# Kernel optimization log

Measured on AMD Instinct MI355X. Metric: run time of the kernel, lower is better.

The kernel has to match this reference:

```python
import jax, jax.numpy as jnp
import numpy as np
from functools import partial

# --- config (matches init_kwargs cfg) ---
MAX_OBS = 16
MAX_AGENTS = 9
NA = MAX_AGENTS - 1            # 8 neighbor agents
NC = MAX_OBS + 2 * NA          # 32 HOCBF constraint rows
A_MAX = 1.0
W_MAX = 1.0
D_MAX = 10.0
D_OBS = 0.5
D_SAFE = 0.5
DAMPING = 2.0
STIFFNESS = 1.0
W_SLACK = 100.0
B = 65536
N_ITERS = 100   # ADMM iterations for the batched QP solve
RHO = 1.0


def setup_inputs() -> dict:
    key = jax.random.key(0)
    k = jax.random.split(key, 8)
    return {
        "u_nominal": jax.random.normal(k[0], (B, 2), dtype=jnp.float32),
        "v_current": jax.random.uniform(k[1], (B, 1), dtype=jnp.float32),
        "p_obs": jax.random.normal(k[2], (B, MAX_OBS, 2), dtype=jnp.float32),
        "p_agents": jax.random.normal(k[3], (B, NA, 2), dtype=jnp.float32),
        "v_agents_local": jax.random.normal(k[4], (B, NA, 2), dtype=jnp.float32),
        "agent_active": jnp.ones((B, NA), dtype=jnp.float32),
        "obs_active": jnp.ones((B, MAX_OBS), dtype=jnp.float32),
    }


def _build_Gh(v_current, p_obs, p_agents, v_agents_local, agent_active, obs_active):
    """Faithful translation of the G/h constraint construction."""
    # obstacle CBF rows  (v_current is (B,1) and broadcasts against (B,MAX_OBS))
    lx_o, ly_o = p_obs[..., 0], p_obs[..., 1]
    h_obs = lx_o ** 2 + ly_o ** 2 - D_OBS ** 2
    h_dot_obs = -2.0 * lx_o * v_current
    G_obs = jnp.stack([2.0 * lx_o,
                       2.0 * ly_o * v_current,
                       -jnp.ones_like(lx_o)], axis=-1)           # (B, MAX_OBS, 3)
    h_obs_row = (2.0 * v_current ** 2 + DAMPING * h_dot_obs
                 + STIFFNESS * h_obs) * obs_active               # (B, MAX_OBS)

    # inter-agent avoidance rows
    lx_a, ly_a = p_agents[..., 0], p_agents[..., 1]
    v_jx, v_jy = v_agents_local[..., 0], v_agents_local[..., 1]
    h_avoid = lx_a ** 2 + ly_a ** 2 - D_SAFE ** 2
    h_dot_avoid = -2.0 * lx_a * v_current + 2.0 * (lx_a * v_jx + ly_a * v_jy)
    G_av_a = 2.0 * lx_a
    G_av_w = 2.0 * ly_a * v_current - 2.0 * ly_a * v_jx + 2.0 * lx_a * v_jy
    h_ddot_c = (2.0 * v_current ** 2 - 2.0 * v_current * v_jx
                + 2.0 * (-v_current * v_jx + v_jx ** 2 + v_jy ** 2))
    G_avoid = jnp.stack([G_av_a * agent_active,
                         G_av_w * agent_active,
                         jnp.zeros_like(lx_a)], axis=-1)         # (B, NA, 3)
    h_avoid_row = (h_ddot_c + DAMPING * h_dot_avoid + STIFFNESS * h_avoid) * agent_active

    # connectivity rows
    h_conn = D_MAX ** 2 - (lx_a ** 2 + ly_a ** 2)
    h_dot_conn = -h_dot_avoid
    G_conn = jnp.stack([-G_av_a * agent_active,
                        -G_av_w * agent_active,
                        jnp.zeros_like(lx_a)], axis=-1)          # (B, NA, 3)
    h_conn_row = (-h_ddot_c + DAMPING * h_dot_conn + STIFFNESS * h_conn) * agent_active

    G = jnp.concatenate([G_obs, G_avoid, G_conn], axis=1)        # (B, NC, 3)
    h = jnp.concatenate([h_obs_row, h_avoid_row, h_conn_row], axis=1)  # (B, NC)
    return G, h


def _solve_qp(u_ref, G, h):
    """Batched ADMM solve of: min ||u - u_ref||^2 + w_slack*delta^2,
    s.t. [G; box] x <= [h; box_b], x = [u1, u2, delta]."""
    Bn = u_ref.shape[0]
    box_A = jnp.array([[-1., 0., 0.], [1., 0., 0.],
                       [0., -1., 0.], [0., 1., 0.],
                       [0., 0., -1.]], dtype=u_ref.dtype)
    box_b = jnp.array([A_MAX, A_MAX, W_MAX, W_MAX, 0.0], dtype=u_ref.dtype)
    A = jnp.concatenate([G, jnp.broadcast_to(box_A, (Bn, 5, 3))], axis=1)  # (B, m, 3)
    b = jnp.concatenate([h, jnp.broadcast_to(box_b, (Bn, 5))], axis=1)     # (B, m)

    Q = jnp.diag(jnp.array([2.0, 2.0, 2.0 * W_SLACK], dtype=u_ref.dtype))
    q = jnp.concatenate([-2.0 * u_ref, jnp.zeros((Bn, 1), u_ref.dtype)], axis=1)

    M = Q + RHO * jnp.einsum('bki,bkj->bij', A, A)   # (B, 3, 3)
    Minv = jnp.linalg.inv(M)

    def step(carry, _):
        x, z, y = carry
        rhs = -q + jnp.einsum('bkj,bk->bj', A, RHO * z - y)
        x = jnp.einsum('bij,bj->bi', Minv, rhs)
        v = jnp.einsum('bkj,bj->bk', A, x)
        z = jnp.minimum(v + y / RHO, b)
        y = y + RHO * (v - z)
        return (x, z, y), None

    x0 = jnp.zeros((Bn, 3), u_ref.dtype)
    z0 = jnp.minimum(jnp.zeros_like(b), b)
    y0 = jnp.zeros_like(b)
    (x, _, _), _ = jax.lax.scan(step, (x0, z0, y0), None, length=N_ITERS)
    return x


def reference(u_nominal, v_current, p_obs, p_agents, v_agents_local,
              agent_active, obs_active):
    action_scale = jnp.array([A_MAX, W_MAX], dtype=u_nominal.dtype)
    u_ref = u_nominal * action_scale
    G, h = _build_Gh(v_current, p_obs, p_agents, v_agents_local,
                     agent_active, obs_active)
    x = _solve_qp(u_ref, G, h)      # (B, 3) = [u1, u2, delta]
    u_safe = x[:, :2] / action_scale
    return u_safe
```

## Files before the change

kernel.cpp:

```cpp
#include <hip/hip_runtime.h>


constexpr int NOBS = 16;
constexpr int NAG  = 8;
constexpr int NITERS = 100;

typedef float v2 __attribute__((ext_vector_type(2)));

static __device__ __forceinline__ v2 vfma(v2 a, v2 b, v2 c) { return __builtin_elementwise_fma(a, b, c); }
static __device__ __forceinline__ v2 vmax(v2 a, v2 b)       { return __builtin_elementwise_max(a, b); }
static __device__ __forceinline__ v2 vabs(v2 a)             { return __builtin_elementwise_abs(a); }

__global__ __launch_bounds__(256, 1)
void cbf_admm_kernel(const float* __restrict__ u_nom,
                     const float* __restrict__ v_cur,
                     const float* __restrict__ p_obs,
                     const float* __restrict__ p_ag,
                     const float* __restrict__ v_ag,
                     const float* __restrict__ ag_act,
                     const float* __restrict__ ob_act,
                     float* __restrict__ out,
                     int B)
{
    const int b = blockIdx.x * blockDim.x + threadIdx.x;
    if (b >= B) return;

    const float v   = v_cur[b];
    const float2 un = *reinterpret_cast<const float2*>(u_nom + 2 * (size_t)b);
    const float ur0 = un.x;
    const float ur1 = un.y;

    v2 ga2[8], gw2[8], h2[8];
    {
        const float4* po = reinterpret_cast<const float4*>(p_obs + (size_t)b * 2 * NOBS);
        const float2* oa = reinterpret_cast<const float2*>(ob_act + (size_t)b * NOBS);
        #pragma unroll
        for (int q = 0; q < 8; ++q) {
            const float4 p  = po[q];
            const float2 ac = oa[q];
            const v2 lx = {p.x, p.z};
            const v2 ly = {p.y, p.w};
            const v2 act = {ac.x, ac.y};
            ga2[q] = 2.f * lx;
            gw2[q] = (2.f * v) * ly;
            const v2 h_obs = lx * lx + ly * ly - 0.25f;
            const v2 hdot  = (-2.f * v) * lx;
            h2[q] = (2.f * v * v + 2.f * hdot + h_obs) * act;
        }
    }

    v2 gaa2[4], gwa2[4], hav2[4], hcn2[4];
    {
        const float4* pa  = reinterpret_cast<const float4*>(p_ag  + (size_t)b * 2 * NAG);
        const float4* va  = reinterpret_cast<const float4*>(v_ag  + (size_t)b * 2 * NAG);
        const float2* aa  = reinterpret_cast<const float2*>(ag_act + (size_t)b * NAG);
        #pragma unroll
        for (int q = 0; q < 4; ++q) {
            const float4 p  = pa[q];
            const float4 w4 = va[q];
            const float2 ac = aa[q];
            const v2 lx = {p.x,  p.z},  ly = {p.y,  p.w};
            const v2 vx = {w4.x, w4.z}, vy = {w4.y, w4.w};
            const v2 act = {ac.x, ac.y};
            const v2 d2  = lx * lx + ly * ly;
            const v2 h_avoid = d2 - 0.25f;
            const v2 hdot = (-2.f * v) * lx + 2.f * (lx * vx + ly * vy);
            const v2 hddc = (2.f * v * v) + (-4.f * v) * vx + 2.f * (vx * vx + vy * vy);
            const v2 Ga = 2.f * lx;
            const v2 Gw = (2.f * v) * ly - 2.f * ly * vx + 2.f * lx * vy;
            gaa2[q] = Ga * act;
            gwa2[q] = Gw * act;
            hav2[q] = (hddc + 2.f * hdot + h_avoid) * act;
            hcn2[q] = (-hddc - 2.f * hdot + (100.f - d2)) * act;
        }
    }

    v2 m00 = {4.f, 0.f}, m01 = {0.f, 0.f}, m11 = {4.f, 0.f}, m02 = {0.f, 0.f}, m12 = {0.f, 0.f};
    #pragma unroll
    for (int q = 0; q < 8; ++q) {
        m00 = vfma(ga2[q], ga2[q], m00);
        m01 = vfma(ga2[q], gw2[q], m01);
        m11 = vfma(gw2[q], gw2[q], m11);
        m02 = m02 - ga2[q];
        m12 = m12 - gw2[q];
    }
    #pragma unroll
    for (int q = 0; q < 4; ++q) {
        const v2 two = {2.f, 2.f};
        m00 = vfma(two * gaa2[q], gaa2[q], m00);
        m01 = vfma(two * gaa2[q], gwa2[q], m01);
        m11 = vfma(two * gwa2[q], gwa2[q], m11);
    }
    const float M00 = m00.x + m00.y, M01 = m01.x + m01.y, M11 = m11.x + m11.y;
    const float M02 = m02.x + m02.y, M12 = m12.x + m12.y;
    const float M22 = 217.f;
    const float c00 = M11 * M22 - M12 * M12;
    const float c01 = M02 * M12 - M01 * M22;
    const float c02 = M01 * M12 - M02 * M11;
    const float det = M00 * c00 + M01 * c01 + M02 * c02;
    const float id  = 1.f / det;
    const float i00 = c00 * id, i01 = c01 * id, i02 = c02 * id;
    const float i11 = (M00 * M22 - M02 * M02) * id;
    const float i12 = (M01 * M02 - M00 * M12) * id;
    const float i22 = (M00 * M11 - M01 * M01) * id;

    const v2 Z = {0.f, 0.f};
    v2 w2[8], wav2[4], wcn2[4];
    #pragma unroll
    for (int q = 0; q < 8; ++q) w2[q] = __builtin_elementwise_min(Z, h2[q]);
    #pragma unroll
    for (int q = 0; q < 4; ++q) {
        wav2[q] = __builtin_elementwise_min(Z, hav2[q]);
        wcn2[q] = __builtin_elementwise_min(Z, hcn2[q]);
    }
    v2 wb01 = Z, wb23 = Z;
    float wb4 = 0.f;
    const v2 ONE = {1.f, 1.f};

    float x0 = 0.f, x1 = 0.f, x2 = 0.f;

    #pragma unroll 1
    for (int it = 0; it < NITERS; ++it) {
        v2 a0 = Z, a1 = Z, a2 = Z;
        v2 dobs[8], dav[4], dcn[4];
        #pragma unroll
        for (int q = 0; q < 8; ++q) {
            const v2 d = w2[q] - h2[q];
            dobs[q] = d;
            const v2 t = h2[q] - vabs(d);
            a0 = vfma(ga2[q], t, a0);
            a1 = vfma(gw2[q], t, a1);
            a2 = a2 - t;
        }
        #pragma unroll
        for (int q = 0; q < 4; ++q) {
            const v2 da = wav2[q] - hav2[q];  dav[q] = da;
            const v2 dc = wcn2[q] - hcn2[q];  dcn[q] = dc;
            const v2 ta = hav2[q] - vabs(da);
            const v2 tc = hcn2[q] - vabs(dc);
            const v2 td = ta - tc;
            a0 = vfma(gaa2[q], td, a0);
            a1 = vfma(gwa2[q], td, a1);
        }
        const v2 db01 = wb01 - ONE, db23 = wb23 - ONE;
        const v2 tb01 = ONE - vabs(db01), tb23 = ONE - vabs(db23);
        const float tb4 = -fabsf(wb4);

        const float r0 = 2.f * ur0 + a0.x + a0.y + (tb01.y - tb01.x);
        const float r1 = 2.f * ur1 + a1.x + a1.y + (tb23.y - tb23.x);
        const float r2 = a2.x + a2.y - tb4;

        x0 = fmaf(i00, r0, fmaf(i01, r1, i02 * r2));
        x1 = fmaf(i01, r0, fmaf(i11, r1, i12 * r2));
        x2 = fmaf(i02, r0, fmaf(i12, r1, i22 * r2));

        const v2 X0 = {x0, x0}, X1 = {x1, x1}, NX2 = {-x2, -x2};
        #pragma unroll
        for (int q = 0; q < 8; ++q) {
            const v2 vv = vfma(ga2[q], X0, vfma(gw2[q], X1, NX2));
            w2[q] = vv + vmax(dobs[q], Z);
        }
        #pragma unroll
        for (int q = 0; q < 4; ++q) {
            const v2 va = vfma(gaa2[q], X0, gwa2[q] * X1);
            wav2[q] = va + vmax(dav[q], Z);
            wcn2[q] = vmax(dcn[q], Z) - va;
        }
        const v2 sx0 = {-x0, x0}, sx1 = {-x1, x1};
        wb01 = sx0 + vmax(db01, Z);
        wb23 = sx1 + vmax(db23, Z);
        wb4  = -x2 + fmaxf(wb4, 0.f);
    }

    reinterpret_cast<float2*>(out)[b] = make_float2(x0, x1);
}

extern "C" void kernel_launch(void* const* d_in, const int* in_sizes, int n_in,
                              void* d_out, int out_size, void* d_ws, size_t ws_size,
                              hipStream_t stream) {
    const float* u_nom  = (const float*)d_in[0];
    const float* v_cur  = (const float*)d_in[1];
    const float* p_obs  = (const float*)d_in[2];
    const float* p_ag   = (const float*)d_in[3];
    const float* v_ag   = (const float*)d_in[4];
    const float* ag_act = (const float*)d_in[5];
    const float* ob_act = (const float*)d_in[6];
    float* out = (float*)d_out;

    const int B = in_sizes[1];
    dim3 block(256), grid((B + 255) / 256);
    hipLaunchKernelGGL(cbf_admm_kernel, grid, block, 0, stream,
                       u_nom, v_cur, p_obs, p_ag, v_ag, ag_act, ob_act, out, B);
}
```

Measured before the change: 49.67 us.

## Split each QP across two lanes with DPP lane-swap reductions

Each batch element is now handled by two adjacent threads, each owning half of the constraint rows. Partial sums for the ADMM right-hand side and the M matrix are combined every iteration with a DPP quad-permute lane swap, and the box constraints are split between the two lanes. Launch bounds move to two blocks per CU and the grid doubles. This is meant to raise parallelism and occupancy for B=65536, since one thread per element gives only 256 blocks. The cost is duplicated 3x3 solve work and a lane exchange on the serial per-iteration dependency chain.

```diff
diff --git a/kernel.cpp b/kernel.cpp
--- a/kernel.cpp
+++ b/kernel.cpp
@@ -1,17 +1,20 @@
 #include <hip/hip_runtime.h>
 
 
-constexpr int NOBS = 16;
-constexpr int NAG  = 8;
 constexpr int NITERS = 100;
 
 typedef float v2 __attribute__((ext_vector_type(2)));
 
 static __device__ __forceinline__ v2 vfma(v2 a, v2 b, v2 c) { return __builtin_elementwise_fma(a, b, c); }
 static __device__ __forceinline__ v2 vmax(v2 a, v2 b)       { return __builtin_elementwise_max(a, b); }
+static __device__ __forceinline__ v2 vmin(v2 a, v2 b)       { return __builtin_elementwise_min(a, b); }
 static __device__ __forceinline__ v2 vabs(v2 a)             { return __builtin_elementwise_abs(a); }
 
-__global__ __launch_bounds__(256, 1)
+static __device__ __forceinline__ float lane_swap(float x) {
+    return __int_as_float(__builtin_amdgcn_mov_dpp(__float_as_int(x), 0xB1, 0xF, 0xF, true));
+}
+
+__global__ __launch_bounds__(256, 2)
 void cbf_admm_kernel(const float* __restrict__ u_nom,
                      const float* __restrict__ v_cur,
                      const float* __restrict__ p_obs,
@@ -22,25 +25,28 @@
                      float* __restrict__ out,
                      int B)
 {
-    const int b = blockIdx.x * blockDim.x + threadIdx.x;
-    if (b >= B) return;
-
-    const float v   = v_cur[b];
-    const float2 un = *reinterpret_cast<const float2*>(u_nom + 2 * (size_t)b);
+    const int t  = blockIdx.x * blockDim.x + threadIdx.x;
+    const int e  = t >> 1;
+    const int hf = t & 1;
+    if (e >= B) return;
+
+    const float v   = v_cur[e];
+    const float2 un = *reinterpret_cast<const float2*>(u_nom + 2 * (size_t)e);
     const float ur0 = un.x;
     const float ur1 = un.y;
 
-    v2 ga2[8], gw2[8], h2[8];
+    v2 ga2[4], gw2[4], h2[4];
     {
-        const float4* po = reinterpret_cast<const float4*>(p_obs + (size_t)b * 2 * NOBS);
-        const float2* oa = reinterpret_cast<const float2*>(ob_act + (size_t)b * NOBS);
-        #pragma unroll
-        for (int q = 0; q < 8; ++q) {
-            const float4 p  = po[q];
-            const float2 ac = oa[q];
+        const float4* po = reinterpret_cast<const float4*>(p_obs) + 4 * (size_t)t;
+        const float4* oa = reinterpret_cast<const float4*>(ob_act) + 2 * (size_t)t;
+        const float4 A0 = oa[0], A1 = oa[1];
+        const float oaf[8] = {A0.x, A0.y, A0.z, A0.w, A1.x, A1.y, A1.z, A1.w};
+        #pragma unroll
+        for (int q = 0; q < 4; ++q) {
+            const float4 p = po[q];
             const v2 lx = {p.x, p.z};
             const v2 ly = {p.y, p.w};
-            const v2 act = {ac.x, ac.y};
+            const v2 act = {oaf[2 * q], oaf[2 * q + 1]};
             ga2[q] = 2.f * lx;
             gw2[q] = (2.f * v) * ly;
             const v2 h_obs = lx * lx + ly * ly - 0.25f;
@@ -49,19 +55,19 @@
         }
     }
 
-    v2 gaa2[4], gwa2[4], hav2[4], hcn2[4];
+    v2 gaa2[2], gwa2[2], hav2[2], hcn2[2];
     {
-        const float4* pa  = reinterpret_cast<const float4*>(p_ag  + (size_t)b * 2 * NAG);
-        const float4* va  = reinterpret_cast<const float4*>(v_ag  + (size_t)b * 2 * NAG);
-        const float2* aa  = reinterpret_cast<const float2*>(ag_act + (size_t)b * NAG);
-        #pragma unroll
-        for (int q = 0; q < 4; ++q) {
+        const float4* pa = reinterpret_cast<const float4*>(p_ag) + 2 * (size_t)t;
+        const float4* va = reinterpret_cast<const float4*>(v_ag) + 2 * (size_t)t;
+        const float4 AA  = reinterpret_cast<const float4*>(ag_act)[t];
+        const float aaf[4] = {AA.x, AA.y, AA.z, AA.w};
+        #pragma unroll
+        for (int q = 0; q < 2; ++q) {
             const float4 p  = pa[q];
             const float4 w4 = va[q];
-            const float2 ac = aa[q];
             const v2 lx = {p.x,  p.z},  ly = {p.y,  p.w};
             const v2 vx = {w4.x, w4.z}, vy = {w4.y, w4.w};
-            const v2 act = {ac.x, ac.y};
+            const v2 act = {aaf[2 * q], aaf[2 * q + 1]};
             const v2 d2  = lx * lx + ly * ly;
             const v2 h_avoid = d2 - 0.25f;
             const v2 hdot = (-2.f * v) * lx + 2.f * (lx * vx + ly * vy);
@@ -75,9 +81,9 @@
         }
     }
 
-    v2 m00 = {4.f, 0.f}, m01 = {0.f, 0.f}, m11 = {4.f, 0.f}, m02 = {0.f, 0.f}, m12 = {0.f, 0.f};
-    #pragma unroll
-    for (int q = 0; q < 8; ++q) {
+    v2 m00 = {0.f, 0.f}, m01 = m00, m11 = m00, m02 = m00, m12 = m00;
+    #pragma unroll
+    for (int q = 0; q < 4; ++q) {
         m00 = vfma(ga2[q], ga2[q], m00);
         m01 = vfma(ga2[q], gw2[q], m01);
         m11 = vfma(gw2[q], gw2[q], m11);
@@ -85,14 +91,19 @@
         m12 = m12 - gw2[q];
     }
     #pragma unroll
-    for (int q = 0; q < 4; ++q) {
-        const v2 two = {2.f, 2.f};
-        m00 = vfma(two * gaa2[q], gaa2[q], m00);
-        m01 = vfma(two * gaa2[q], gwa2[q], m01);
-        m11 = vfma(two * gwa2[q], gwa2[q], m11);
-    }
-    const float M00 = m00.x + m00.y, M01 = m01.x + m01.y, M11 = m11.x + m11.y;
-    const float M02 = m02.x + m02.y, M12 = m12.x + m12.y;
+    for (int q = 0; q < 2; ++q) {
+        const v2 g2 = gaa2[q] + gaa2[q];
+        m00 = vfma(g2, gaa2[q], m00);
+        m01 = vfma(g2, gwa2[q], m01);
+        m11 = vfma(gwa2[q] + gwa2[q], gwa2[q], m11);
+    }
+    float pM00 = m00.x + m00.y, pM01 = m01.x + m01.y, pM11 = m11.x + m11.y;
+    float pM02 = m02.x + m02.y, pM12 = m12.x + m12.y;
+    const float M00 = pM00 + lane_swap(pM00) + 4.f;
+    const float M01 = pM01 + lane_swap(pM01);
+    const float M11 = pM11 + lane_swap(pM11) + 4.f;
+    const float M02 = pM02 + lane_swap(pM02);
+    const float M12 = pM12 + lane_swap(pM12);
     const float M22 = 217.f;
     const float c00 = M11 * M22 - M12 * M12;
     const float c01 = M02 * M12 - M01 * M22;
@@ -105,35 +116,35 @@
     const float i22 = (M00 * M11 - M01 * M01) * id;
 
     const v2 Z = {0.f, 0.f};
-    v2 w2[8], wav2[4], wcn2[4];
-    #pragma unroll
-    for (int q = 0; q < 8; ++q) w2[q] = __builtin_elementwise_min(Z, h2[q]);
-    #pragma unroll
-    for (int q = 0; q < 4; ++q) {
-        wav2[q] = __builtin_elementwise_min(Z, hav2[q]);
-        wcn2[q] = __builtin_elementwise_min(Z, hcn2[q]);
-    }
-    v2 wb01 = Z, wb23 = Z;
+    const v2 ONE = {1.f, 1.f};
+    v2 w2[4], wav2[2], wcn2[2];
+    #pragma unroll
+    for (int q = 0; q < 4; ++q) w2[q] = vmin(Z, h2[q]);
+    #pragma unroll
+    for (int q = 0; q < 2; ++q) {
+        wav2[q] = vmin(Z, hav2[q]);
+        wcn2[q] = vmin(Z, hcn2[q]);
+    }
+    v2 wbp = Z;
     float wb4 = 0.f;
-    const v2 ONE = {1.f, 1.f};
 
     float x0 = 0.f, x1 = 0.f, x2 = 0.f;
 
     #pragma unroll 1
     for (int it = 0; it < NITERS; ++it) {
-        v2 a0 = Z, a1 = Z, a2 = Z;
-        v2 dobs[8], dav[4], dcn[4];
-        #pragma unroll
-        for (int q = 0; q < 8; ++q) {
+        v2 a0 = Z, a1 = Z, tsum = Z;
+        v2 dobs[4], dav[2], dcn[2];
+        #pragma unroll
+        for (int q = 0; q < 4; ++q) {
             const v2 d = w2[q] - h2[q];
             dobs[q] = d;
-            const v2 t = h2[q] - vabs(d);
-            a0 = vfma(ga2[q], t, a0);
-            a1 = vfma(gw2[q], t, a1);
-            a2 = a2 - t;
-        }
-        #pragma unroll
-        for (int q = 0; q < 4; ++q) {
+            const v2 tt = h2[q] - vabs(d);
+            a0 = vfma(ga2[q], tt, a0);
+            a1 = vfma(gw2[q], tt, a1);
+            tsum = tsum + tt;
+        }
+        #pragma unroll
+        for (int q = 0; q < 2; ++q) {
             const v2 da = wav2[q] - hav2[q];  dav[q] = da;
             const v2 dc = wcn2[q] - hcn2[q];  dcn[q] = dc;
             const v2 ta = hav2[q] - vabs(da);
@@ -142,13 +153,20 @@
             a0 = vfma(gaa2[q], td, a0);
             a1 = vfma(gwa2[q], td, a1);
         }
-        const v2 db01 = wb01 - ONE, db23 = wb23 - ONE;
-        const v2 tb01 = ONE - vabs(db01), tb23 = ONE - vabs(db23);
-        const float tb4 = -fabsf(wb4);
-
-        const float r0 = 2.f * ur0 + a0.x + a0.y + (tb01.y - tb01.x);
-        const float r1 = 2.f * ur1 + a1.x + a1.y + (tb23.y - tb23.x);
-        const float r2 = a2.x + a2.y - tb4;
+        const v2 db = wbp - ONE;
+        const v2 tb = ONE - vabs(db);
+        const float rbox = tb.y - tb.x;
+
+        float p0 = a0.x + a0.y;
+        float p1 = a1.x + a1.y;
+        float p2 = -(tsum.x + tsum.y);
+        p0 += hf ? 0.f : rbox;
+        p1 += hf ? rbox : 0.f;
+        p2 += hf ? 0.f : fabsf(wb4);
+
+        const float r0 = p0 + lane_swap(p0) + 2.f * ur0;
+        const float r1 = p1 + lane_swap(p1) + 2.f * ur1;
+        const float r2 = p2 + lane_swap(p2);
 
         x0 = fmaf(i00, r0, fmaf(i01, r1, i02 * r2));
         x1 = fmaf(i01, r0, fmaf(i11, r1, i12 * r2));
@@ -156,23 +174,24 @@
 
         const v2 X0 = {x0, x0}, X1 = {x1, x1}, NX2 = {-x2, -x2};
         #pragma unroll
-        for (int q = 0; q < 8; ++q) {
+        for (int q = 0; q < 4; ++q) {
             const v2 vv = vfma(ga2[q], X0, vfma(gw2[q], X1, NX2));
             w2[q] = vv + vmax(dobs[q], Z);
         }
         #pragma unroll
-        for (int q = 0; q < 4; ++q) {
-            const v2 va = vfma(gaa2[q], X0, gwa2[q] * X1);
-            wav2[q] = va + vmax(dav[q], Z);
-            wcn2[q] = vmax(dcn[q], Z) - va;
-        }
-        const v2 sx0 = {-x0, x0}, sx1 = {-x1, x1};
-        wb01 = sx0 + vmax(db01, Z);
-        wb23 = sx1 + vmax(db23, Z);
-        wb4  = -x2 + fmaxf(wb4, 0.f);
-    }
-
-    reinterpret_cast<float2*>(out)[b] = make_float2(x0, x1);
+        for (int q = 0; q < 2; ++q) {
+            const v2 va_ = vfma(gaa2[q], X0, gwa2[q] * X1);
+            wav2[q] = va_ + vmax(dav[q], Z);
+            wcn2[q] = vmax(dcn[q], Z) - va_;
+        }
+        const float xsel = hf ? x1 : x0;
+        const v2 sx = {-xsel, xsel};
+        wbp = sx + vmax(db, Z);
+        wb4 = -x2 + fmaxf(wb4, 0.f);
+    }
+
+    if (hf == 0)
+        reinterpret_cast<float2*>(out)[e] = make_float2(x0, x1);
 }
 
 extern "C" void kernel_launch(void* const* d_in, const int* in_sizes, int n_in,
@@ -188,7 +207,8 @@
     float* out = (float*)d_out;
 
     const int B = in_sizes[1];
-    dim3 block(256), grid((B + 255) / 256);
+    const int threads = 2 * B;
+    dim3 block(256), grid((threads + 255) / 256);
     hipLaunchKernelGGL(cbf_admm_kernel, grid, block, 0, stream,
                        u_nom, v_cur, p_obs, p_ag, v_ag, ag_act, ob_act, out, B);
 }
```

Measured after the change: 49.52 us. About the same (-0.3%).
